# Kernel tuning notes

Hardware: AMD Instinct MI355X
Metric: run time of the kernel (lower is better)

The kernel has to match this reference:

```python
import jax, jax.numpy as jnp
import numpy as np

EPS = 1e-6
REP = 28  # hardcoded expand factor in the original module: bs = 28 * time_stamp


def setup_inputs() -> dict:
    key = jax.random.key(0)
    k1, k2, k3, k4, k5 = jax.random.split(key, 5)
    T, N, E0, E1, IN_FT, OUT_FT = 8, 1024, 256, 256, 64, 64
    bs = REP * T
    x = jax.random.normal(k1, (bs, N, IN_FT), dtype=jnp.float32)
    G = jax.random.uniform(k2, (N, E0), dtype=jnp.float32)
    G1 = jax.random.uniform(k3, (T, N, E1), dtype=jnp.float32)
    stdv = 1.0 / np.sqrt(OUT_FT)
    weight = jax.random.uniform(k4, (IN_FT, OUT_FT), dtype=jnp.float32, minval=-stdv, maxval=stdv)
    bias = jax.random.uniform(k5, (OUT_FT,), dtype=jnp.float32, minval=-stdv, maxval=stdv)
    return {"x": x, "G": G, "G1": G1, "weight": weight, "bias": bias}


def reference(x, G, G1, weight, bias):
    T, N, _ = G1.shape
    bs = x.shape[0]
    # G_combined: static incidence broadcast over time, concat with dynamic part -> [T, N, E]
    Gc = jnp.concatenate([jnp.broadcast_to(G[None], (T,) + G.shape), G1], axis=-1)
    # Diagonal degree matrices -> just vectors; inv(sqrt(Dv)) and inv(De) are elementwise.
    dv_inv_sqrt = 1.0 / jnp.sqrt(Gc.sum(axis=2) + EPS)   # [T, N]
    de_inv = 1.0 / (Gc.sum(axis=1) + EPS)                # [T, E]
    # L = Dv^{-1/2} G De^{-1} G^T Dv^{-1/2}  -> [T, N, N]
    A = Gc * de_inv[:, None, :]
    L = dv_inv_sqrt[:, :, None] * jnp.einsum('tne,tme->tnm', A, Gc) * dv_inv_sqrt[:, None, :]
    # x @ W + b, then apply per-timestep Laplacian (each L repeated REP times along batch)
    xw = x @ weight + bias                                # [bs, N, F]
    F = xw.shape[-1]
    xw_t = xw.reshape(T, bs // T, N, F)
    out = jnp.einsum('tnm,tbmf->tbnf', L, xw_t).reshape(bs, N, F)
    return out
```

## Files before the change

### kernel.cpp

```cpp
#include <hip/hip_runtime.h>
#include <hip/hip_bf16.h>
#include <stdint.h>

typedef __bf16 bf16x8 __attribute__((ext_vector_type(8)));
typedef float f32x4 __attribute__((ext_vector_type(4)));
typedef unsigned short u16;

#define EPS_ 1e-6f

__device__ __forceinline__ void gload16(const void* g, void* l) {
  __builtin_amdgcn_global_load_lds((const __attribute__((address_space(1))) void*)g,
                                   (__attribute__((address_space(3))) void*)l,
                                   16, 0, 0);
}

__device__ __forceinline__ u16 f2bf(float v) {
  __hip_bfloat16 h = __float2bfloat16(v);
  return *reinterpret_cast<u16*>(&h);
}

__global__ void dv_kernel(const float* __restrict__ G, const float* __restrict__ G1,
                          float* __restrict__ dv) {
  const int row = blockIdx.x * 4 + (threadIdx.x >> 6);
  const int lane = threadIdx.x & 63;
  const int t = row >> 10, n = row & 1023;
  const float4 g  = ((const float4*)(G  + (size_t)n * 256))[lane];
  const float4 g1 = ((const float4*)(G1 + ((size_t)t * 1024 + n) * 256))[lane];
  float s = g.x + g.y + g.z + g.w + g1.x + g1.y + g1.z + g1.w;
  #pragma unroll
  for (int off = 1; off < 64; off <<= 1) s += __shfl_xor(s, off);
  if (lane == 0) dv[row] = rsqrtf(s + EPS_);
}

__global__ void de_partial_kernel(const float* __restrict__ G, const float* __restrict__ G1,
                                  float* __restrict__ dep) {
  const int t = blockIdx.x >> 4;
  const int c = blockIdx.x & 15;
  const int e = threadIdx.x;
  const int n0 = c * 64;
  float s = 0.0f;
  if (e < 256) {
    const float* p = G + (size_t)n0 * 256 + e;
    #pragma unroll 8
    for (int n = 0; n < 64; ++n) s += p[(size_t)n * 256];
  } else {
    const float* p = G1 + ((size_t)t * 1024 + n0) * 256 + (e - 256);
    #pragma unroll 8
    for (int n = 0; n < 64; ++n) s += p[(size_t)n * 256];
  }
  dep[(size_t)blockIdx.x * 512 + e] = s;
}

__global__ void de_final_kernel(const float* __restrict__ dep, float* __restrict__ de) {
  const int t = blockIdx.x;
  const int e = threadIdx.x;
  float s = 0.0f;
  #pragma unroll
  for (int c = 0; c < 16; ++c) s += dep[(size_t)(t * 16 + c) * 512 + e];
  de[t * 512 + e] = rsqrtf(s + EPS_);
}

__global__ void pack_kernel(const float* __restrict__ G, const float* __restrict__ G1,
                            const float* __restrict__ dv, const float* __restrict__ de,
                            u16* __restrict__ P) {
  const int idx = blockIdx.x * 256 + threadIdx.x;
  const int e4 = idx & 127;
  const int n  = (idx >> 7) & 1023;
  const int t  = idx >> 17;
  const int e  = e4 * 4;
  float4 g;
  if (e < 256) g = *(const float4*)(G + (size_t)n * 256 + e);
  else         g = *(const float4*)(G1 + ((size_t)t * 1024 + n) * 256 + (e - 256));
  const float4 d = *(const float4*)(de + t * 512 + e);
  const float dvn = dv[t * 1024 + n];
  u16 o[4];
  o[0] = f2bf(g.x * d.x * dvn);
  o[1] = f2bf(g.y * d.y * dvn);
  o[2] = f2bf(g.z * d.z * dvn);
  o[3] = f2bf(g.w * d.w * dvn);
  *(ushort4*)(P + ((size_t)t * 1024 + n) * 512 + e) = *(ushort4*)o;
}

__global__ __launch_bounds__(256) void xwt_mfma_kernel(
    const float* __restrict__ x, const float* __restrict__ w,
    const float* __restrict__ bias, u16* __restrict__ xt) {
  __shared__ u16 As[256 * 72];
  __shared__ u16 WT[64 * 136];
  const int tid = threadIdx.x;
  const int tb = blockIdx.x >> 2;
  const int m0 = (blockIdx.x & 3) * 256;
  const size_t r0 = (size_t)tb * 1024 + m0;

  {
    const int f = tid & 63, kq = tid >> 6;
    #pragma unroll
    for (int kk = 0; kk < 16; ++kk) {
      const int k = kq * 16 + kk;
      const float wv = w[k * 64 + f];
      const float hf = __bfloat162float(__float2bfloat16(wv));
      WT[f * 136 + k]      = f2bf(wv);
      WT[f * 136 + 64 + k] = f2bf(wv - hf);
    }
  }
  {
    const float4* xb = (const float4*)(x + r0 * 64);
    #pragma unroll
    for (int i = 0; i < 16; ++i) {
      const int fi = tid + i * 256;
      const int row = fi >> 4, c4 = fi & 15;
      const float4 v = xb[fi];
      ushort4 o = { f2bf(v.x), f2bf(v.y), f2bf(v.z), f2bf(v.w) };
      *(ushort4*)&As[row * 72 + c4 * 4] = o;
    }
  }
  __syncthreads();

  const int lane = tid & 63, wv_ = tid >> 6;
  const int c = lane & 15, q = lane >> 4;

  bf16x8 a[4][2], bf_[4][4];
  #pragma unroll
  for (int i = 0; i < 4; ++i)
    #pragma unroll
    for (int s = 0; s < 2; ++s)
      a[i][s] = *(const bf16x8*)&As[(wv_ * 64 + i * 16 + c) * 72 + s * 32 + q * 8];
  #pragma unroll
  for (int j = 0; j < 4; ++j)
    #pragma unroll
    for (int s = 0; s < 4; ++s)
      bf_[j][s] = *(const bf16x8*)&WT[(j * 16 + c) * 136 + s * 32 + q * 8];

  f32x4 acc[4][4];
  #pragma unroll
  for (int j = 0; j < 4; ++j) {
    const float bv = bias[j * 16 + c];
    #pragma unroll
    for (int i = 0; i < 4; ++i) acc[i][j] = { bv, bv, bv, bv };
  }
  #pragma unroll
  for (int i = 0; i < 4; ++i)
    #pragma unroll
    for (int j = 0; j < 4; ++j) {
      acc[i][j] = __builtin_amdgcn_mfma_f32_16x16x32_bf16(a[i][0], bf_[j][0], acc[i][j], 0, 0, 0);
      acc[i][j] = __builtin_amdgcn_mfma_f32_16x16x32_bf16(a[i][1], bf_[j][1], acc[i][j], 0, 0, 0);
      acc[i][j] = __builtin_amdgcn_mfma_f32_16x16x32_bf16(a[i][0], bf_[j][2], acc[i][j], 0, 0, 0);
      acc[i][j] = __builtin_amdgcn_mfma_f32_16x16x32_bf16(a[i][1], bf_[j][3], acc[i][j], 0, 0, 0);
    }

  u16* xtb = xt + (size_t)tb * 64 * 1024 + m0;
  #pragma unroll
  for (int j = 0; j < 4; ++j) {
    const int f = j * 16 + c;
    #pragma unroll
    for (int i = 0; i < 4; ++i) {
      const int mr = wv_ * 64 + i * 16 + q * 4;
      ushort4 o = { f2bf(acc[i][j][0]), f2bf(acc[i][j][1]),
                    f2bf(acc[i][j][2]), f2bf(acc[i][j][3]) };
      *(ushort4*)&xtb[(size_t)f * 1024 + mr] = o;
    }
  }
}

template <int K, int MODE, int CHUNK>
__global__ __launch_bounds__(256) void gemm_bt_kernel(
    const u16* __restrict__ Abase, const u16* __restrict__ Bbase,
    u16* __restrict__ Lw, float* __restrict__ Oo) {
  const int wg = (blockIdx.x & 7) * CHUNK + (blockIdx.x >> 3);
  const int t = wg / CHUNK;
  const int bx = wg - t * CHUNK;
  const int row0 = (bx & 7) * 128;
  const int col0 = (bx >> 3) * 128;
  const size_t aoff = (MODE == 0) ? (size_t)t * 1024 * 512 : (size_t)t * 1024 * 1024;
  const size_t boff = (MODE == 0) ? (size_t)t * 1024 * 512 : (size_t)t * 1792 * 1024;
  const u16* A = Abase + aoff;
  const u16* B = Bbase + boff;

  __shared__ u16 As[128 * 32];
  __shared__ u16 Bs[128 * 32];

  const int tid = threadIdx.x;
  const int lane = tid & 63;
  const int wave = tid >> 6;
  const int wr = wave & 1, wc = wave >> 1;

  const int srow = tid >> 2;
  const int scol = (tid & 3) * 8;

  f32x4 acc[4][4] = {};

  const int l16 = lane & 15;
  const int lk = (lane >> 4) * 8;

  for (int kt = 0; kt < K / 32; ++kt) {
    const int kk = kt * 32 + scol;
    gload16(A + (size_t)(row0 + srow) * K + kk,       &As[srow * 32 + scol]);
    gload16(A + (size_t)(row0 + srow + 64) * K + kk,  &As[(srow + 64) * 32 + scol]);
    gload16(B + (size_t)(col0 + srow) * K + kk,       &Bs[srow * 32 + scol]);
    gload16(B + (size_t)(col0 + srow + 64) * K + kk,  &Bs[(srow + 64) * 32 + scol]);
    __syncthreads();
    bf16x8 af[4], bfr[4];
    #pragma unroll
    for (int i = 0; i < 4; ++i) {
      af[i]  = *(const bf16x8*)&As[(wr * 64 + i * 16 + l16) * 32 + lk];
      bfr[i] = *(const bf16x8*)&Bs[(wc * 64 + i * 16 + l16) * 32 + lk];
    }
    #pragma unroll
    for (int i = 0; i < 4; ++i)
      #pragma unroll
      for (int j = 0; j < 4; ++j)
        acc[i][j] = __builtin_amdgcn_mfma_f32_16x16x32_bf16(af[i], bfr[j], acc[i][j], 0, 0, 0);
    __syncthreads();
  }

  const int l4 = lane >> 4;
  if constexpr (MODE == 0) {
    u16* Lt = Lw + (size_t)t * 1024 * 1024;
    #pragma unroll
    for (int i = 0; i < 4; ++i) {
      const int rbase = row0 + wr * 64 + i * 16 + l4 * 4;
      #pragma unroll
      for (int j = 0; j < 4; ++j) {
        const int col = col0 + wc * 64 + j * 16 + l16;
        #pragma unroll
        for (int r = 0; r < 4; ++r)
          Lt[(size_t)(rbase + r) * 1024 + col] = f2bf(acc[i][j][r]);
      }
    }
  } else {
    #pragma unroll
    for (int j = 0; j < 4; ++j) {
      const int jg = col0 + wc * 64 + j * 16 + l16;
      float* Ot = Oo + (((size_t)t * 28 + (jg >> 6)) * 1024) * 64 + (jg & 63);
      #pragma unroll
      for (int i = 0; i < 4; ++i) {
        const int rbase = row0 + wr * 64 + i * 16 + l4 * 4;
        #pragma unroll
        for (int r = 0; r < 4; ++r)
          Ot[(size_t)(rbase + r) * 64] = acc[i][j][r];
      }
    }
  }
}

extern "C" void kernel_launch(void* const* d_in, const int* in_sizes, int n_in,
                              void* d_out, int out_size, void* d_ws, size_t ws_size,
                              hipStream_t stream) {
  const float* x  = (const float*)d_in[0];
  const float* G  = (const float*)d_in[1];
  const float* G1 = (const float*)d_in[2];
  const float* W  = (const float*)d_in[3];
  const float* Bi = (const float*)d_in[4];
  float* out = (float*)d_out;

  char* ws = (char*)d_ws;
  float* dv = (float*)ws;
  float* de = (float*)(ws + 32768);
  u16*   P  = (u16*)(ws + 49152);
  u16*   L  = (u16*)(ws + 49152 + 8388608);
  u16*   XT = (u16*)(ws + 49152 + 8388608 + 16777216);
  float* dep = (float*)L;

  dv_kernel<<<2048, 256, 0, stream>>>(G, G1, dv);
  de_partial_kernel<<<128, 512, 0, stream>>>(G, G1, dep);
  de_final_kernel<<<8, 512, 0, stream>>>(dep, de);
  pack_kernel<<<4096, 256, 0, stream>>>(G, G1, dv, de, P);
  gemm_bt_kernel<512, 0, 64><<<512, 256, 0, stream>>>(P, P, L, nullptr);
  xwt_mfma_kernel<<<896, 256, 0, stream>>>(x, W, Bi, XT);
  gemm_bt_kernel<1024, 1, 112><<<896, 256, 0, stream>>>(L, XT, nullptr, out);
}
```

Measured before the change: 197.8 us.

## Double GEMM K-tile to 64 and XOR-swizzle LDS layout

Each main-loop iteration of the bf16 MFMA GEMM now covers 64 of K instead of 32, which halves the number of barrier pairs and loop iterations. Both LDS tiles double in size. The LDS layout is XOR-swizzled on 16-byte chunks by row, applied to the global source address because global_load_lds writes contiguously, so that fragment reads avoid bank conflicts. The cost is more LDS per block, which may reduce occupancy, and there is still no double buffering.

```diff
diff --git a/kernel.cpp b/kernel.cpp
--- a/kernel.cpp
+++ b/kernel.cpp
@@ -175,44 +175,57 @@
   const u16* A = Abase + aoff;
   const u16* B = Bbase + boff;
 
-  __shared__ u16 As[128 * 32];
-  __shared__ u16 Bs[128 * 32];
+  __shared__ u16 As[128 * 64];
+  __shared__ u16 Bs[128 * 64];
 
   const int tid = threadIdx.x;
   const int lane = tid & 63;
   const int wave = tid >> 6;
   const int wr = wave & 1, wc = wave >> 1;
 
-  const int srow = tid >> 2;
-  const int scol = (tid & 3) * 8;
+  const int srow8 = tid >> 3;
+  const int schunk = tid & 7;
 
   f32x4 acc[4][4] = {};
 
   const int l16 = lane & 15;
-  const int lk = (lane >> 4) * 8;
-
-  for (int kt = 0; kt < K / 32; ++kt) {
-    const int kk = kt * 32 + scol;
-    gload16(A + (size_t)(row0 + srow) * K + kk,       &As[srow * 32 + scol]);
-    gload16(A + (size_t)(row0 + srow + 64) * K + kk,  &As[(srow + 64) * 32 + scol]);
-    gload16(B + (size_t)(col0 + srow) * K + kk,       &Bs[srow * 32 + scol]);
-    gload16(B + (size_t)(col0 + srow + 64) * K + kk,  &Bs[(srow + 64) * 32 + scol]);
+  const int q = lane >> 4;
+
+  for (int kt = 0; kt < K / 64; ++kt) {
+    const int kk0 = kt * 64;
+    #pragma unroll
+    for (int i = 0; i < 4; ++i) {
+      const int row = i * 32 + srow8;
+      const int csrc = schunk ^ (row & 7);
+      gload16(A + (size_t)(row0 + row) * K + kk0 + csrc * 8, &As[row * 64 + schunk * 8]);
+      gload16(B + (size_t)(col0 + row) * K + kk0 + csrc * 8, &Bs[row * 64 + schunk * 8]);
+    }
     __syncthreads();
-    bf16x8 af[4], bfr[4];
-    #pragma unroll
-    for (int i = 0; i < 4; ++i) {
-      af[i]  = *(const bf16x8*)&As[(wr * 64 + i * 16 + l16) * 32 + lk];
-      bfr[i] = *(const bf16x8*)&Bs[(wc * 64 + i * 16 + l16) * 32 + lk];
+
+    bf16x8 af[4][2], bfr[4][2];
+    #pragma unroll
+    for (int i = 0; i < 4; ++i) {
+      const int ar = wr * 64 + i * 16 + l16;
+      const int br = wc * 64 + i * 16 + l16;
+      #pragma unroll
+      for (int h = 0; h < 2; ++h) {
+        const int ca = (h * 4 + q) ^ (ar & 7);
+        const int cb = (h * 4 + q) ^ (br & 7);
+        af[i][h]  = *(const bf16x8*)&As[ar * 64 + ca * 8];
+        bfr[i][h] = *(const bf16x8*)&Bs[br * 64 + cb * 8];
+      }
     }
     #pragma unroll
     for (int i = 0; i < 4; ++i)
       #pragma unroll
-      for (int j = 0; j < 4; ++j)
-        acc[i][j] = __builtin_amdgcn_mfma_f32_16x16x32_bf16(af[i], bfr[j], acc[i][j], 0, 0, 0);
+      for (int j = 0; j < 4; ++j) {
+        acc[i][j] = __builtin_amdgcn_mfma_f32_16x16x32_bf16(af[i][0], bfr[j][0], acc[i][j], 0, 0, 0);
+        acc[i][j] = __builtin_amdgcn_mfma_f32_16x16x32_bf16(af[i][1], bfr[j][1], acc[i][j], 0, 0, 0);
+      }
     __syncthreads();
   }
 
-  const int l4 = lane >> 4;
+  const int l4 = q;
   if constexpr (MODE == 0) {
     u16* Lt = Lw + (size_t)t * 1024 * 1024;
     #pragma unroll
```

Result: faster. 190.0 us (-4.0%).
